# Kernel tuning notes

Measured on AMD Instinct MI355X. Metric: run time of the kernel, lower is better.

Reference implementation:

```python
import jax, jax.numpy as jnp
import numpy as np

NUM_HEADS = 12


def setup_inputs() -> dict:
    key = jax.random.key(0)
    ks = jax.random.split(key, 6)
    B, N, C = 16, 576, 768
    H, D = NUM_HEADS, 768 // NUM_HEADS
    P = 16
    x = jax.random.normal(ks[0], (B, N, C), dtype=jnp.float32)
    prompt = jax.random.normal(ks[1], (B, 2, P, H, D), dtype=jnp.float32)
    act_scale = jax.random.uniform(ks[2], (2,), dtype=jnp.float32)
    qkv_w = jax.random.normal(ks[3], (3 * C, C), dtype=jnp.float32) * (C ** -0.5)
    proj_w = jax.random.normal(ks[4], (C, C), dtype=jnp.float32) * (C ** -0.5)
    proj_b = jnp.zeros((C,), dtype=jnp.float32)
    return {"x": x, "prompt": prompt, "act_scale": act_scale,
            "qkv_w": qkv_w, "proj_w": proj_w, "proj_b": proj_b}


def reference(x, prompt, act_scale, qkv_w, proj_w, proj_b):
    B, N, C = x.shape
    H = NUM_HEADS
    D = C // H
    scale = D ** -0.5
    # qkv projection: [B,N,3C] -> (3,B,H,N,D)
    qkv = (x @ qkv_w.T).reshape(B, N, 3, H, D).transpose(2, 0, 3, 1, 4)
    q, k, v = qkv[0], qkv[1], qkv[2]
    # prompt: [B,2,P,H,D] -> (2,B,H,P,D)
    pr = jnp.transpose(prompt, (1, 0, 3, 2, 4))
    key_prefix, value_prefix = pr[0], pr[1]        # [B,H,P,D]
    v = jnp.concatenate([value_prefix, v], axis=2)  # [B,H,P+N,D]
    # gated prefix scores
    prompt_attn = jnp.einsum('bhnd,bhpd->bhnp', q, key_prefix) * scale
    prompt_attn = prompt_attn + jnp.tanh(prompt_attn * act_scale[0]) * act_scale[1]
    # standard scores
    attn = jnp.einsum('bhnd,bhmd->bhnm', q, k) * scale
    attn = jnp.concatenate([prompt_attn, attn], axis=-1)  # [B,H,N,P+N]
    attn = jax.nn.softmax(attn, axis=-1)
    out = jnp.einsum('bhnm,bhmd->bhnd', attn, v)  # [B,H,N,D]
    out = out.transpose(0, 2, 1, 3).reshape(B, N, C)
    return out @ proj_w.T + proj_b
```

## Files before the change

### kernel.cpp

```cpp
#include <hip/hip_runtime.h>
#include <hip/hip_bf16.h>
#include <math.h>

namespace {

constexpr int kB = 16, kN = 576, kC = 768, kH = 12, kP = 16;
constexpr int kM = kB * kN;

typedef __attribute__((ext_vector_type(8))) __bf16 bf16x8;
typedef __attribute__((ext_vector_type(4))) float  f32x4;
typedef __attribute__((ext_vector_type(8))) unsigned short u16x8;

__device__ inline unsigned short f2bf(float f) {
  __bf16 h = (__bf16)f;
  return __builtin_bit_cast(unsigned short, h);
}
__device__ inline float bf2f(unsigned short u) {
  unsigned int x = ((unsigned int)u) << 16;
  return __builtin_bit_cast(float, x);
}
__device__ inline unsigned int pk2bf(float lo, float hi) {
  return (unsigned int)f2bf(lo) | ((unsigned int)f2bf(hi) << 16);
}
__device__ inline int xcd_swz(int hw, int nwg) {
  const int per = nwg >> 3;
  return (hw & 7) * per + (hw >> 3);
}

#define GLDS16(src, dst) __builtin_amdgcn_global_load_lds( \
    (const __attribute__((address_space(1))) unsigned int*)(src), \
    (__attribute__((address_space(3))) unsigned int*)(dst), 16, 0, 0)

__global__ __launch_bounds__(256)
void cvt3(const float* __restrict__ x, const float* __restrict__ wq,
          const float* __restrict__ wp, unsigned short* __restrict__ xo,
          unsigned short* __restrict__ wqo, unsigned short* __restrict__ wpo) {
  const int bid = blockIdx.x;
  const float* in; unsigned short* out; int base;
  if (bid < 6912)       { in = x;  out = xo;  base = bid; }
  else if (bid < 8640)  { in = wq; out = wqo; base = bid - 6912; }
  else                  { in = wp; out = wpo; base = bid - 8640; }
  const int i = base * 256 + threadIdx.x;
  const float4 v = ((const float4*)in)[i];
  ((ushort4*)out)[i] = make_ushort4(f2bf(v.x), f2bf(v.y), f2bf(v.z), f2bf(v.w));
}

template<int OB>
__global__ __launch_bounds__(256)
void gemm_bf16(const unsigned short* __restrict__ A, const unsigned short* __restrict__ W,
               const float* __restrict__ bias, void* __restrict__ Yv, int Kd, int Nd) {
  __shared__ __align__(16) unsigned short As[2][8192];
  __shared__ __align__(16) unsigned short Bs[2][8192];
  const int tid  = threadIdx.x;
  const int wv   = tid >> 6, lane = tid & 63;
  const int gx   = Nd >> 7;
  const int lg   = xcd_swz(blockIdx.x, gridDim.x);
  const long bm  = (long)(lg / gx) * 128;
  const long bn  = (long)(lg % gx) * 128;
  const int wr   = (wv >> 1) * 64;
  const int wc   = (wv & 1) * 64;
  const int row15 = lane & 15, kg = lane >> 4;

  auto stage = [&](int buf, int kt) {
#pragma unroll
    for (int site = 0; site < 4; ++site) {
      const int u = site * 256 + tid;
      const int row = u >> 3, slot = u & 7;
      const int ksw = kt + (((slot ^ (row & 7)) << 3));
      GLDS16(A + (bm + row) * (long)Kd + ksw, &As[buf][site * 2048 + wv * 512]);
      GLDS16(W + (bn + row) * (long)Kd + ksw, &Bs[buf][site * 2048 + wv * 512]);
    }
  };

  float bvpre[4] = {0.0f, 0.0f, 0.0f, 0.0f};
  if constexpr (!OB) {
#pragma unroll
    for (int ni = 0; ni < 4; ++ni) bvpre[ni] = bias[bn + wc + ni * 16 + row15];
  }
  asm volatile("s_waitcnt vmcnt(0)" ::: "memory");

  f32x4 acc[4][4] = {};
  stage(0, 0);

  const int sw8 = row15 & 7;
  const int nt = Kd >> 6;
  for (int t = 0; t < nt; ++t) {
    const int cur = t & 1;
    __builtin_amdgcn_sched_barrier(0);
    __builtin_amdgcn_s_barrier();
    if (t + 1 < nt) stage(cur ^ 1, (t + 1) << 6);
    if (t + 1 < nt)      asm volatile("s_waitcnt vmcnt(8)");
    else                 asm volatile("s_waitcnt vmcnt(0)");
    __builtin_amdgcn_s_barrier();
    __builtin_amdgcn_sched_barrier(0);

    bf16x8 af[4][2], bf_[4][2];
#pragma unroll
    for (int mi = 0; mi < 4; ++mi)
#pragma unroll
      for (int ks = 0; ks < 2; ++ks)
        af[mi][ks] = *(const bf16x8*)(&As[cur][(wr + mi * 16 + row15) * 64 +
                                               (((ks * 4 + kg) ^ sw8) << 3)]);
#pragma unroll
    for (int ni = 0; ni < 4; ++ni)
#pragma unroll
      for (int ks = 0; ks < 2; ++ks)
        bf_[ni][ks] = *(const bf16x8*)(&Bs[cur][(wc + ni * 16 + row15) * 64 +
                                                (((ks * 4 + kg) ^ sw8) << 3)]);
    __builtin_amdgcn_s_setprio(1);
#pragma unroll
    for (int ks = 0; ks < 2; ++ks)
#pragma unroll
      for (int mi = 0; mi < 4; ++mi)
#pragma unroll
        for (int ni = 0; ni < 4; ++ni)
          acc[mi][ni] = __builtin_amdgcn_mfma_f32_16x16x32_bf16(af[mi][ks], bf_[ni][ks],
                                                                acc[mi][ni], 0, 0, 0);
    __builtin_amdgcn_s_setprio(0);
  }

  const int r4 = kg * 4;
#pragma unroll
  for (int ni = 0; ni < 4; ++ni) {
    const long col = bn + wc + ni * 16 + row15;
    if constexpr (OB) {
      unsigned short* Y = (unsigned short*)Yv;
#pragma unroll
      for (int mi = 0; mi < 4; ++mi)
#pragma unroll
        for (int j = 0; j < 4; ++j)
          Y[(bm + wr + mi * 16 + r4 + j) * (long)Nd + col] = f2bf(acc[mi][ni][j]);
    } else {
      float* Y = (float*)Yv;
#pragma unroll
      for (int mi = 0; mi < 4; ++mi)
#pragma unroll
        for (int j = 0; j < 4; ++j)
          Y[(bm + wr + mi * 16 + r4 + j) * (long)Nd + col] = acc[mi][ni][j] + bvpre[ni];
    }
  }
}

__device__ inline void softmax_group_static(f32x4 (&c)[4], float& lsum,
                                            unsigned short* pl,
                                            const int kg, const int sw) {
  float psum = 0.0f;
#pragma unroll
  for (int kb = 0; kb < 4; ++kb) {
    const float p0 = __expf(c[kb][0] - 10.0f);
    const float p1 = __expf(c[kb][1] - 10.0f);
    const float p2 = __expf(c[kb][2] - 10.0f);
    const float p3 = __expf(c[kb][3] - 10.0f);
    psum += (p0 + p1) + (p2 + p3);
    const int off = (((kb * 2 + (kg >> 1)) ^ sw) << 3) + (kg & 1) * 4;
    *(uint2*)(pl + off) = make_uint2(pk2bf(p0, p1), pk2bf(p2, p3));
  }
  lsum += psum;
}

__global__ __launch_bounds__(192, 3)
void attn_mfma(const unsigned short* __restrict__ qkv, const float* __restrict__ prompt,
               const float* __restrict__ act_scale, unsigned short* __restrict__ attn_out) {
  const int lg = xcd_swz(blockIdx.x, gridDim.x);
  const int qt = lg % 6, bh = lg / 6;
  const int h = bh % kH, b = bh / kH;
  const int tid = threadIdx.x, wv = tid >> 6, lane = tid & 63;
  const int q15 = lane & 15, kg = lane >> 4;

  __shared__ __align__(16) unsigned short Klds[2][4096];
  __shared__ __align__(16) unsigned short Vt[2][4096];
  __shared__ __align__(16) unsigned short Plds[3][2048];

  const float a0 = act_scale[0], a1 = act_scale[1];
  const int sw  = q15 & 7;
  const int sl0 = (kg ^ sw) << 3;
  const int sl1 = ((4 + kg) ^ sw) << 3;

  bf16x8 qf[2][2];
#pragma unroll
  for (int g = 0; g < 2; ++g) {
    const unsigned short* qrow =
        qkv + (size_t)(b * kN + qt * 96 + wv * 32 + g * 16 + q15) * 2304 + h * 64;
#pragma unroll
    for (int dh = 0; dh < 2; ++dh) {
      u16x8 raw = *(const u16x8*)(qrow + dh * 32 + kg * 8);
      u16x8 sc;
#pragma unroll
      for (int j = 0; j < 8; ++j) sc[j] = f2bf(bf2f(raw[j]) * 0.125f);
      qf[g][dh] = __builtin_bit_cast(bf16x8, sc);
    }
  }

  if (tid < 128) {
    const int r = tid >> 3, s = tid & 7;
    const float* src = prompt + (((size_t)(b * 2) * kP + r) * kH + h) * 64 + s * 8;
    const f32x4 f0 = *(const f32x4*)src, f1 = *(const f32x4*)(src + 4);
    *(uint4*)(&Klds[0][r * 64 + ((s ^ (r & 7)) << 3)]) =
        make_uint4(pk2bf(f0[0], f0[1]), pk2bf(f0[2], f0[3]),
                   pk2bf(f1[0], f1[1]), pk2bf(f1[2], f1[3]));
  }
  if (tid < 128) {
    const int kp = tid & 7, vdq = tid >> 3;
    const float* s0 = prompt + (((size_t)(b * 2 + 1) * kP + 2 * kp) * kH + h) * 64 + vdq * 4;
    const f32x4 x0 = *(const f32x4*)s0;
    const f32x4 y0 = *(const f32x4*)(s0 + kH * 64);
#pragma unroll
    for (int j = 0; j < 4; ++j) {
      const int d = vdq * 4 + j;
      *(unsigned int*)(&Vt[0][d * 64 + (((kp >> 2) ^ (d & 7)) << 3) + (kp & 3) * 2]) =
          pk2bf(x0[j], y0[j]);
    }
  }
#pragma unroll
  for (int i = 0; i < 2; ++i) {
    const int idx = tid + 192 * i;
    const int d = idx / 6, szl = (idx % 6) + 2;
    *(uint4*)(&Vt[0][d * 64 + ((szl ^ (d & 7)) << 3)]) = make_uint4(0, 0, 0, 0);
  }
  __syncthreads();

  f32x4 o0[4] = {}, o1[4] = {};
  float l0 = 0.0f, l1 = 0.0f;

  const int vkp  = tid & 31;
  const int vdgb = tid >> 5;
  const int kr8  = lane >> 3, ks8 = lane & 7;

  for (int ch = 0; ch < 10; ++ch) {
    const int cur = ch & 1;

    u16x8 va0, va1, vb0, vb1;
    const bool doV = (ch < 9) && (wv < 2);
    if (ch < 9) {
      if (doV) {
        const unsigned short* r0 = qkv + (size_t)(b * kN + ch * 64 + 2 * vkp) * 2304 + 1536 + h * 64;
        va0 = *(const u16x8*)(r0 + vdgb * 8);
        va1 = *(const u16x8*)(r0 + (vdgb + 4) * 8);
        vb0 = *(const u16x8*)(r0 + 2304 + vdgb * 8);
        vb1 = *(const u16x8*)(r0 + 2304 + (vdgb + 4) * 8);
      } else if (wv == 2) {
#pragma unroll
        for (int g8 = 0; g8 < 8; ++g8) {
          const int r = g8 * 8 + kr8;
          const unsigned short* src =
              qkv + (size_t)(b * kN + ch * 64 + r) * 2304 + 768 + h * 64 + ((ks8 ^ (r & 7)) << 3);
          GLDS16(src, &Klds[cur ^ 1][g8 * 512]);
        }
      }
    }

    f32x4 c0[4], c1[4];
    __builtin_amdgcn_s_setprio(1);
#pragma unroll
    for (int kb = 0; kb < 4; ++kb) {
      if (ch == 0 && kb > 0) {
        c0[kb][0] = c0[kb][1] = c0[kb][2] = c0[kb][3] = -1.0e30f;
        c1[kb][0] = c1[kb][1] = c1[kb][2] = c1[kb][3] = -1.0e30f;
      } else {
        const unsigned short* krow = &Klds[cur][(kb * 16 + q15) * 64];
        const bf16x8 k0 = *(const bf16x8*)(krow + sl0);
        const bf16x8 k1 = *(const bf16x8*)(krow + sl1);
        f32x4 t0 = {}, t1 = {};
        t0 = __builtin_amdgcn_mfma_f32_16x16x32_bf16(k0, qf[0][0], t0, 0, 0, 0);
        c0[kb] = __builtin_amdgcn_mfma_f32_16x16x32_bf16(k1, qf[0][1], t0, 0, 0, 0);
        t1 = __builtin_amdgcn_mfma_f32_16x16x32_bf16(k0, qf[1][0], t1, 0, 0, 0);
        c1[kb] = __builtin_amdgcn_mfma_f32_16x16x32_bf16(k1, qf[1][1], t1, 0, 0, 0);
      }
    }
    __builtin_amdgcn_s_setprio(0);
    if (ch == 0) {
#pragma unroll
      for (int j = 0; j < 4; ++j) {
        const float s0v = c0[0][j];
        const float e0 = __expf(2.0f * s0v * a0);
        c0[0][j] = s0v + ((e0 - 1.0f) / (e0 + 1.0f)) * a1;
        const float s1v = c1[0][j];
        const float e1 = __expf(2.0f * s1v * a0);
        c1[0][j] = s1v + ((e1 - 1.0f) / (e1 + 1.0f)) * a1;
      }
    }

    softmax_group_static(c0, l0, &Plds[wv][q15 * 64], kg, sw);
    softmax_group_static(c1, l1, &Plds[wv][(q15 + 16) * 64], kg, sw);

    if (doV) {
#pragma unroll
      for (int j = 0; j < 8; ++j) {
        const int d0 = vdgb * 8 + j;
        *(unsigned int*)(&Vt[cur ^ 1][d0 * 64 + (((vkp >> 2) ^ (d0 & 7)) << 3) + (vkp & 3) * 2]) =
            (unsigned int)va0[j] | ((unsigned int)vb0[j] << 16);
        const int d1 = (vdgb + 4) * 8 + j;
        *(unsigned int*)(&Vt[cur ^ 1][d1 * 64 + (((vkp >> 2) ^ (d1 & 7)) << 3) + (vkp & 3) * 2]) =
            (unsigned int)va1[j] | ((unsigned int)vb1[j] << 16);
      }
    }

    const unsigned short* p0 = &Plds[wv][q15 * 64];
    const unsigned short* p1 = &Plds[wv][(q15 + 16) * 64];
    const bf16x8 pa00 = *(const bf16x8*)(p0 + sl0);
    const bf16x8 pa01 = *(const bf16x8*)(p0 + sl1);
    const bf16x8 pa10 = *(const bf16x8*)(p1 + sl0);
    const bf16x8 pa11 = *(const bf16x8*)(p1 + sl1);
    __builtin_amdgcn_s_setprio(1);
#pragma unroll
    for (int nb = 0; nb < 4; ++nb) {
      const unsigned short* vr = &Vt[cur][(nb * 16 + q15) * 64];
      const bf16x8 bv0 = *(const bf16x8*)(vr + sl0);
      const bf16x8 bv1 = *(const bf16x8*)(vr + sl1);
      o0[nb] = __builtin_amdgcn_mfma_f32_16x16x32_bf16(pa00, bv0, o0[nb], 0, 0, 0);
      o0[nb] = __builtin_amdgcn_mfma_f32_16x16x32_bf16(pa01, bv1, o0[nb], 0, 0, 0);
      o1[nb] = __builtin_amdgcn_mfma_f32_16x16x32_bf16(pa10, bv0, o1[nb], 0, 0, 0);
      o1[nb] = __builtin_amdgcn_mfma_f32_16x16x32_bf16(pa11, bv1, o1[nb], 0, 0, 0);
    }
    __builtin_amdgcn_s_setprio(0);

    __syncthreads();
  }

  l0 += __shfl_xor(l0, 16, 64);
  l0 += __shfl_xor(l0, 32, 64);
  l1 += __shfl_xor(l1, 16, 64);
  l1 += __shfl_xor(l1, 32, 64);
  const float i0 = 1.0f / l0, i1 = 1.0f / l1;
  float iq0[4], iq1[4];
#pragma unroll
  for (int jr = 0; jr < 4; ++jr) {
    iq0[jr] = __shfl(i0, kg * 4 + jr, 64);
    iq1[jr] = __shfl(i1, kg * 4 + jr, 64);
  }
  unsigned short* ob = attn_out + (size_t)(b * kN + qt * 96 + wv * 32) * 768 + h * 64;
#pragma unroll
  for (int nb = 0; nb < 4; ++nb)
#pragma unroll
    for (int jr = 0; jr < 4; ++jr) {
      ob[(size_t)(kg * 4 + jr) * 768 + nb * 16 + q15] = f2bf(o0[nb][jr] * iq0[jr]);
      ob[(size_t)(16 + kg * 4 + jr) * 768 + nb * 16 + q15] = f2bf(o1[nb][jr] * iq1[jr]);
    }
}

}

extern "C" void kernel_launch(void* const* d_in, const int* in_sizes, int n_in,
                              void* d_out, int out_size, void* d_ws, size_t ws_size,
                              hipStream_t stream) {
  const float* x         = (const float*)d_in[0];
  const float* prompt    = (const float*)d_in[1];
  const float* act_scale = (const float*)d_in[2];
  const float* qkv_w     = (const float*)d_in[3];
  const float* proj_w    = (const float*)d_in[4];
  const float* proj_b    = (const float*)d_in[5];
  float* out = (float*)d_out;

  char* ws = (char*)d_ws;
  unsigned short* qkvb   = (unsigned short*)ws;
  unsigned short* xa     = (unsigned short*)(ws + 42467328);
  unsigned short* qkvwb  = (unsigned short*)(ws + 42467328 + 14155776);
  unsigned short* projwb = (unsigned short*)(ws + 42467328 + 14155776 + 3538944);

  cvt3<<<9216, 256, 0, stream>>>(x, qkv_w, proj_w, xa, qkvwb, projwb);

  gemm_bf16<1><<<(3 * kC / 128) * (kM / 128), 256, 0, stream>>>(xa, qkvwb, nullptr, qkvb, kC, 3 * kC);
  attn_mfma<<<(kN / 96) * kH * kB, 192, 0, stream>>>(qkvb, prompt, act_scale, xa);
  gemm_bf16<0><<<(kC / 128) * (kM / 128), 256, 0, stream>>>(xa, projwb, proj_b, out, kC, kC);
}
```

Measured before the change: 119.5 us.

## Replace double-buffered direct-to-LDS loads with register-staged single-buffer GEMM pipeline

The GEMM mainloop stops using double-buffered global-to-LDS direct loads and instead prefetches the next K tile into registers, computes on a single LDS buffer, then writes the registers into LDS after a barrier. This halves the LDS footprint, which could raise occupancy, and overlaps global loads with MFMA compute through registers. In exchange it adds VGPR pressure, an extra LDS write pass, and two full barriers per iteration in place of the hand-tuned waitcnt scheme.

```diff
diff --git a/kernel.cpp b/kernel.cpp
--- a/kernel.cpp
+++ b/kernel.cpp
@@ -49,8 +49,8 @@
 __global__ __launch_bounds__(256)
 void gemm_bf16(const unsigned short* __restrict__ A, const unsigned short* __restrict__ W,
                const float* __restrict__ bias, void* __restrict__ Yv, int Kd, int Nd) {
-  __shared__ __align__(16) unsigned short As[2][8192];
-  __shared__ __align__(16) unsigned short Bs[2][8192];
+  __shared__ __align__(16) unsigned short As[8192];
+  __shared__ __align__(16) unsigned short Bs[8192];
   const int tid  = threadIdx.x;
   const int wv   = tid >> 6, lane = tid & 63;
   const int gx   = Nd >> 7;
@@ -61,14 +61,24 @@
   const int wc   = (wv & 1) * 64;
   const int row15 = lane & 15, kg = lane >> 4;
 
-  auto stage = [&](int buf, int kt) {
+  u16x8 ra[4], rb[4];
+  auto loadregs = [&](int kt) {
 #pragma unroll
     for (int site = 0; site < 4; ++site) {
       const int u = site * 256 + tid;
       const int row = u >> 3, slot = u & 7;
-      const int ksw = kt + (((slot ^ (row & 7)) << 3));
-      GLDS16(A + (bm + row) * (long)Kd + ksw, &As[buf][site * 2048 + wv * 512]);
-      GLDS16(W + (bn + row) * (long)Kd + ksw, &Bs[buf][site * 2048 + wv * 512]);
+      ra[site] = *(const u16x8*)(A + (bm + row) * (long)Kd + kt + slot * 8);
+      rb[site] = *(const u16x8*)(W + (bn + row) * (long)Kd + kt + slot * 8);
+    }
+  };
+  auto writeLDS = [&]() {
+#pragma unroll
+    for (int site = 0; site < 4; ++site) {
+      const int u = site * 256 + tid;
+      const int row = u >> 3, slot = u & 7;
+      const int off = row * 64 + ((slot ^ (row & 7)) << 3);
+      *(u16x8*)(As + off) = ra[site];
+      *(u16x8*)(Bs + off) = rb[site];
     }
   };
 
@@ -77,36 +87,30 @@
 #pragma unroll
     for (int ni = 0; ni < 4; ++ni) bvpre[ni] = bias[bn + wc + ni * 16 + row15];
   }
-  asm volatile("s_waitcnt vmcnt(0)" ::: "memory");
 
   f32x4 acc[4][4] = {};
-  stage(0, 0);
+  loadregs(0);
+  writeLDS();
 
   const int sw8 = row15 & 7;
   const int nt = Kd >> 6;
   for (int t = 0; t < nt; ++t) {
-    const int cur = t & 1;
-    __builtin_amdgcn_sched_barrier(0);
-    __builtin_amdgcn_s_barrier();
-    if (t + 1 < nt) stage(cur ^ 1, (t + 1) << 6);
-    if (t + 1 < nt)      asm volatile("s_waitcnt vmcnt(8)");
-    else                 asm volatile("s_waitcnt vmcnt(0)");
-    __builtin_amdgcn_s_barrier();
-    __builtin_amdgcn_sched_barrier(0);
+    __syncthreads();
+    if (t + 1 < nt) loadregs((t + 1) << 6);
 
     bf16x8 af[4][2], bf_[4][2];
 #pragma unroll
     for (int mi = 0; mi < 4; ++mi)
 #pragma unroll
       for (int ks = 0; ks < 2; ++ks)
-        af[mi][ks] = *(const bf16x8*)(&As[cur][(wr + mi * 16 + row15) * 64 +
-                                               (((ks * 4 + kg) ^ sw8) << 3)]);
+        af[mi][ks] = *(const bf16x8*)(&As[(wr + mi * 16 + row15) * 64 +
+                                          (((ks * 4 + kg) ^ sw8) << 3)]);
 #pragma unroll
     for (int ni = 0; ni < 4; ++ni)
 #pragma unroll
       for (int ks = 0; ks < 2; ++ks)
-        bf_[ni][ks] = *(const bf16x8*)(&Bs[cur][(wc + ni * 16 + row15) * 64 +
-                                                (((ks * 4 + kg) ^ sw8) << 3)]);
+        bf_[ni][ks] = *(const bf16x8*)(&Bs[(wc + ni * 16 + row15) * 64 +
+                                           (((ks * 4 + kg) ^ sw8) << 3)]);
     __builtin_amdgcn_s_setprio(1);
 #pragma unroll
     for (int ks = 0; ks < 2; ++ks)
@@ -117,6 +121,8 @@
           acc[mi][ni] = __builtin_amdgcn_mfma_f32_16x16x32_bf16(af[mi][ks], bf_[ni][ks],
                                                                 acc[mi][ni], 0, 0, 0);
     __builtin_amdgcn_s_setprio(0);
+    __syncthreads();
+    if (t + 1 < nt) writeLDS();
   }
 
   const int r4 = kg * 4;
```

Measured after the change: 118.7 us, median of 2. No clear change (-0.7%).
